# Kernel optimization log

Hardware: AMD Instinct MI355X
Metric: run time of the kernel (lower is better)

Reference implementation:

```python
import jax, jax.numpy as jnp
import numpy as np

N = 50000; E = 320000; DIN = 768; D = 256; R = 4; L = 3
B = 64; T = 6; SD = 128; SH = 256; NC = 14; ALPHA = 0.15
NEG = -1e30


def setup_inputs():
    keys = iter(jax.random.split(jax.random.key(0), 64))
    def nrm(shape, s=0.02):
        return s * jax.random.normal(next(keys), shape, dtype=jnp.float32)
    inp = {}
    inp["x"] = jax.random.normal(next(keys), (N, DIN), dtype=jnp.float32)
    inp["edge_index"] = jax.random.randint(next(keys), (2, E), 0, N)
    inp["edge_type"] = jax.random.randint(next(keys), (E,), 0, R)
    inp["batch"] = jnp.sort(jax.random.randint(next(keys), (N,), 0, B))
    inp["sequence"] = jax.random.normal(next(keys), (B, T, SD), dtype=jnp.float32)
    inp["proj_W"] = nrm((D, DIN)); inp["proj_b"] = nrm((D,))
    inp["Wr"] = nrm((L, R, D, D))
    inp["Ws"] = nrm((L, D, D)); inp["bs"] = nrm((L, D))
    inp["att_W1"] = nrm((L, R, D // 2, 2 * D)); inp["att_b1"] = nrm((L, R, D // 2))
    inp["att_W2"] = nrm((L, R, D // 2)); inp["att_b2"] = nrm((L, R))
    inp["emb"] = nrm((L, R, D // 4), 0.1)
    inp["imp"] = jnp.tile(jnp.array([1.2, 1.1, 1.4, 0.9], dtype=jnp.float32), (L, 1))
    inp["ln_g"] = jnp.ones((L, D), jnp.float32); inp["ln_b"] = jnp.zeros((L, D), jnp.float32)
    inp["gm_W1"] = nrm((D // 2, D)); inp["gm_b1"] = nrm((D // 2,))
    inp["gm_W2"] = nrm((D // 4, D // 2)); inp["gm_b2"] = nrm((D // 4,))
    inp["gm_W3"] = nrm((NC, D // 4)); inp["gm_b3"] = nrm((NC,))
    inp["gru_Wih"] = nrm((2, 3 * SH, SD)); inp["gru_Whh"] = nrm((2, 3 * SH, SH))
    inp["gru_bih"] = nrm((2, 3 * SH)); inp["gru_bhh"] = nrm((2, 3 * SH))
    inp["sm_W1"] = nrm((SH, 2 * SH)); inp["sm_b1"] = nrm((SH,))
    inp["sm_W2"] = nrm((SH // 2, SH)); inp["sm_b2"] = nrm((SH // 2,))
    inp["sm_W3"] = nrm((NC, SH // 2)); inp["sm_b3"] = nrm((NC,))
    return inp


def _gru_dir(x, Wih, Whh, bih, bhh):  # x: [B,T,SD] -> [B,T,SH], torch GRU equations
    def step(h, xt):
        gi = xt @ Wih.T + bih
        gh = h @ Whh.T + bhh
        ir, iz, in_ = jnp.split(gi, 3, axis=-1)
        hr, hz, hn = jnp.split(gh, 3, axis=-1)
        r = jax.nn.sigmoid(ir + hr)
        z = jax.nn.sigmoid(iz + hz)
        n = jnp.tanh(in_ + r * hn)
        h = (1.0 - z) * n + z * h
        return h, h
    h0 = jnp.zeros((x.shape[0], Whh.shape[1]), x.dtype)
    _, ys = jax.lax.scan(step, h0, jnp.swapaxes(x, 0, 1))
    return jnp.swapaxes(ys, 0, 1)


def _gnn_layer(h, h0, src, dst, et, Wr, Ws, bs, aW1, ab1, aW2, ab2, emb, imp, g, b):
    ew = jax.nn.softmax(imp)  # layer_edge_importance softmax over R types
    cat = jnp.concatenate([h[dst], h[src]], axis=1)  # [E, 2D] = [x_i, x_j]
    agg = jnp.zeros_like(h)
    for r in range(R):
        tx = h @ Wr[r].T  # [N, D] per-type transform
        s = jax.nn.relu(cat @ aW1[r].T + ab1[r]) @ aW2[r] + ab2[r]  # [E]
        s = jax.nn.leaky_relu(s, 0.2) + jnp.mean(emb[r])
        mask = et == r
        a = jax.nn.softmax(jnp.where(mask, s, NEG))  # softmax over all type-r edges (dim=0 in torch)
        a = jnp.where(mask, a, 0.0)
        msg = jax.ops.segment_sum(a[:, None] * tx[src], dst, num_segments=h.shape[0])
        agg = agg + ew[r] * msg
    out = (1.0 - ALPHA) * agg + h @ Ws.T + bs + ALPHA * h0
    mu = jnp.mean(out, axis=-1, keepdims=True)
    var = jnp.var(out, axis=-1, keepdims=True)
    out = (out - mu) / jnp.sqrt(var + 1e-5) * g + b  # LayerNorm (eps=1e-5)
    return jax.nn.gelu(out, approximate=False)


def _forward(x, sequence, proj_W, proj_b, Wr, Ws, bs, att_W1, att_b1, att_W2, att_b2, emb, imp, ln_g, ln_b, gm_W1, gm_b1, gm_W2, gm_b2, gm_W3, gm_b3, gru_Wih, gru_Whh, gru_bih, gru_bhh, sm_W1, sm_b1, sm_W2, sm_b2, sm_W3, sm_b3, edge_index, edge_type, batch):
    # sequence branch: bidirectional GRU, avg+max pool over time, MLP readout
    fwd = _gru_dir(sequence, gru_Wih[0], gru_Whh[0], gru_bih[0], gru_bhh[0])
    bwd = _gru_dir(sequence[:, ::-1], gru_Wih[1], gru_Whh[1], gru_bih[1], gru_bhh[1])[:, ::-1]
    seq_out = jnp.concatenate([fwd, bwd], axis=-1)  # [B, T, 2*SH]
    z = jnp.mean(seq_out, axis=1) + jnp.max(seq_out, axis=1)
    z = jax.nn.relu(z @ sm_W1.T + sm_b1)
    z = jax.nn.relu(z @ sm_W2.T + sm_b2)
    seq_logits = z @ sm_W3.T + sm_b3
    # graph branch
    src, dst = edge_index[0], edge_index[1]
    h = x @ proj_W.T + proj_b
    h0 = h
    for i in range(L):
        h = _gnn_layer(h, h0, src, dst, edge_type, Wr[i], Ws[i], bs[i], att_W1[i], att_b1[i], att_W2[i], att_b2[i], emb[i], imp[i], ln_g[i], ln_b[i])
    sums = jax.ops.segment_sum(h, batch, num_segments=B)
    cnt = jax.ops.segment_sum(jnp.ones((h.shape[0],), h.dtype), batch, num_segments=B)
    pooled = sums / jnp.clip(cnt, 1.0)[:, None]  # global_mean_pool
    gz = jax.nn.relu(pooled @ gm_W1.T + gm_b1)
    gz = jax.nn.relu(gz @ gm_W2.T + gm_b2)
    graph_logits = gz @ gm_W3.T + gm_b3
    return graph_logits + seq_logits


def reference(x, edge_index, edge_type, batch, sequence, proj_W, proj_b, Wr, Ws, bs, att_W1, att_b1, att_W2, att_b2, emb, imp, ln_g, ln_b, gm_W1, gm_b1, gm_W2, gm_b2, gm_W3, gm_b3, gru_Wih, gru_Whh, gru_bih, gru_bhh, sm_W1, sm_b1, sm_W2, sm_b2, sm_W3, sm_b3):
    return _forward(x, sequence, proj_W, proj_b, Wr, Ws, bs, att_W1, att_b1, att_W2, att_b2, emb, imp, ln_g, ln_b, gm_W1, gm_b1, gm_W2, gm_b2, gm_W3, gm_b3, gru_Wih, gru_Whh, gru_bih, gru_bhh, sm_W1, sm_b1, sm_W2, sm_b2, sm_W3, sm_b3, edge_index, edge_type, batch)
```

## Files before the change

### kernel.cpp

```cpp
#include <hip/hip_runtime.h>
#include <math.h>

#define N_NODES 50000
#define E_EDGES 320000
#define DIN_    768
#define D_      256
#define R_TYPES 4
#define L_LAYERS 3
#define BATCH_  64
#define T_STEPS 6
#define SD_     128
#define SH_     256
#define NC_     14
#define ALPHA_  0.15f
#define NBLK_B  1250
#define POOL_CHUNK 256
#define E_PAD   (E_EDGES + 256)
#define SCAN_BLK 49

typedef __bf16 bf16_t;
typedef bf16_t bf16x8_t __attribute__((ext_vector_type(8)));
typedef bf16_t bf16x4_t __attribute__((ext_vector_type(4)));
typedef float  f32x4_t  __attribute__((ext_vector_type(4)));

__device__ __forceinline__ f32x4_t mfma16(bf16x8_t a, bf16x8_t b, f32x4_t c) {
    return __builtin_amdgcn_mfma_f32_16x16x32_bf16(a, b, c, 0, 0, 0);
}

__global__ void f2b_kernel(const float* __restrict__ src, bf16_t* __restrict__ dst, int n4)
{
    for (int i = blockIdx.x * blockDim.x + threadIdx.x; i < n4; i += gridDim.x * blockDim.x) {
        float4 v = ((const float4*)src)[i];
        bf16_t o[4] = {(bf16_t)v.x, (bf16_t)v.y, (bf16_t)v.z, (bf16_t)v.w};
        *(ulong1*)&dst[i * 4] = *(ulong1*)o;
    }
}

__global__ void transpose2_kernel(const float* __restrict__ in, float* __restrict__ out, int R, int C)
{
    int total = 2 * R * C;
    for (int i = blockIdx.x * blockDim.x + threadIdx.x; i < total; i += gridDim.x * blockDim.x) {
        int dir = i / (R * C);
        int rem = i - dir * R * C;
        int r = rem / C, c = rem - r * C;
        out[dir * R * C + c * R + r] = in[i];
    }
}

template <bool AF32>
__global__ __launch_bounds__(256) void linear_mfma_t(
    const void* __restrict__ Aptr, const bf16_t* __restrict__ W,
    const float* __restrict__ bias, float* __restrict__ outf,
    bf16_t* __restrict__ outb, int M, int K, int N)
{
    __shared__ bf16_t As[64][40];
    __shared__ bf16_t Bs[64][40];
    const int m0 = blockIdx.x * 64;
    const int n0 = blockIdx.y * 64;
    const int tid = threadIdx.x;
    const int wave = tid >> 6, lane = tid & 63;
    const int wy = wave >> 1, wx = wave & 1;
    const int q = lane >> 4, c = lane & 15;
    const int srow = tid >> 2, skq = tid & 3;

    f32x4_t acc[2][2] = {};
    for (int k0 = 0; k0 < K; k0 += 32) {
        {
            int m = m0 + srow;
            if (AF32) {
                const float* A = (const float*)Aptr;
                bf16_t tmp[8] = {};
                if (m < M) {
                    float4 v0 = *(const float4*)&A[(size_t)m * K + k0 + skq * 8];
                    float4 v1 = *(const float4*)&A[(size_t)m * K + k0 + skq * 8 + 4];
                    tmp[0] = (bf16_t)v0.x; tmp[1] = (bf16_t)v0.y; tmp[2] = (bf16_t)v0.z; tmp[3] = (bf16_t)v0.w;
                    tmp[4] = (bf16_t)v1.x; tmp[5] = (bf16_t)v1.y; tmp[6] = (bf16_t)v1.z; tmp[7] = (bf16_t)v1.w;
                }
                *(bf16x8_t*)&As[srow][skq * 8] = *(bf16x8_t*)tmp;
            } else {
                const bf16_t* A = (const bf16_t*)Aptr;
                bf16x8_t av = {};
                if (m < M) av = *(const bf16x8_t*)&A[(size_t)m * K + k0 + skq * 8];
                *(bf16x8_t*)&As[srow][skq * 8] = av;
            }
            *(bf16x8_t*)&Bs[srow][skq * 8] = *(const bf16x8_t*)&W[(size_t)(n0 + srow) * K + k0 + skq * 8];
        }
        __syncthreads();
        bf16x8_t af[2], bfv[2];
        #pragma unroll
        for (int mt = 0; mt < 2; mt++) af[mt] = *(const bf16x8_t*)&As[wy * 32 + mt * 16 + c][q * 8];
        #pragma unroll
        for (int nt = 0; nt < 2; nt++) bfv[nt] = *(const bf16x8_t*)&Bs[wx * 32 + nt * 16 + c][q * 8];
        #pragma unroll
        for (int mt = 0; mt < 2; mt++)
            #pragma unroll
            for (int nt = 0; nt < 2; nt++)
                acc[mt][nt] = mfma16(af[mt], bfv[nt], acc[mt][nt]);
        __syncthreads();
    }
    #pragma unroll
    for (int mt = 0; mt < 2; mt++) {
        #pragma unroll
        for (int nt = 0; nt < 2; nt++) {
            int n = n0 + wx * 32 + nt * 16 + c;
            float bv = bias ? bias[n] : 0.0f;
            #pragma unroll
            for (int j = 0; j < 4; j++) {
                int m = m0 + wy * 32 + mt * 16 + q * 4 + j;
                if (m < M) {
                    float v = acc[mt][nt][j] + bv;
                    if (outf) outf[(size_t)m * N + n] = v;
                    if (outb) outb[(size_t)m * N + n] = (bf16_t)v;
                }
            }
        }
    }
}

__global__ __launch_bounds__(256) void bucket_count2(const int* __restrict__ et,
                                                     int* __restrict__ blockCnt)
{
    int b = blockIdx.x, tid = threadIdx.x;
    int r = et[b * 256 + tid];
    int lane = tid & 63, wv = tid >> 6;
    __shared__ int wcnt[4][4];
    #pragma unroll
    for (int t = 0; t < 4; t++) {
        unsigned long long m = __ballot(r == t);
        if (lane == 0) wcnt[wv][t] = __popcll(m);
    }
    __syncthreads();
    if (tid < 4)
        blockCnt[b * 4 + tid] = wcnt[0][tid] + wcnt[1][tid] + wcnt[2][tid] + wcnt[3][tid];
}

__global__ void bucket_scan(const int* __restrict__ blockCnt, int* __restrict__ boffP,
                            int* __restrict__ cnt, int* __restrict__ basePerBlock,
                            int* __restrict__ bsrc, int* __restrict__ bdst)
{
    __shared__ int tot[4];
    int t = threadIdx.x;
    if (t < 4) {
        int s = 0;
        for (int b = 0; b < NBLK_B; b++) s += blockCnt[b * 4 + t];
        tot[t] = s;
    }
    __syncthreads();
    if (t == 0) {
        int o = 0;
        for (int r = 0; r < 4; r++) {
            boffP[r] = o; cnt[r] = tot[r];
            o += (tot[r] + 63) & ~63;
        }
        boffP[4] = o;
    }
    __syncthreads();
    if (t < 4) {
        int run = boffP[t];
        for (int b = 0; b < NBLK_B; b++) { basePerBlock[b * 4 + t] = run; run += blockCnt[b * 4 + t]; }
    }
    __syncthreads();
    for (int r = 0; r < 4; r++) {
        int s = boffP[r] + cnt[r], e = boffP[r + 1];
        for (int i = s + t; i < e; i += 64) { bsrc[i] = 0; bdst[i] = 0; }
    }
}

__global__ __launch_bounds__(256) void bucket_scatter2(
    const int* __restrict__ ei, const int* __restrict__ et,
    const int* __restrict__ basePerBlock, int* __restrict__ bsrc, int* __restrict__ bdst)
{
    int b = blockIdx.x, tid = threadIdx.x;
    int e = b * 256 + tid;
    int r = et[e];
    int lane = tid & 63, wv = tid >> 6;
    __shared__ int wcnt[4][4];
    int myrank = 0;
    unsigned long long ltmask = (1ull << lane) - 1ull;
    #pragma unroll
    for (int t = 0; t < 4; t++) {
        unsigned long long m = __ballot(r == t);
        if (r == t) myrank = __popcll(m & ltmask);
        if (lane == 0) wcnt[wv][t] = __popcll(m);
    }
    __syncthreads();
    int wbase = 0;
    for (int w = 0; w < wv; w++) wbase += wcnt[w][r];
    int pos = basePerBlock[b * 4 + r] + wbase + myrank;
    bsrc[pos] = ei[e];
    bdst[pos] = ei[E_EDGES + e];
}

__global__ void embmean_kernel(const float* __restrict__ emb, float* __restrict__ em)
{
    int lr = threadIdx.x;
    if (lr < L_LAYERS * R_TYPES) {
        float s = 0.0f;
        for (int k = 0; k < 64; k++) s += emb[lr * 64 + k];
        em[lr] = s / 64.0f;
    }
}

__global__ __launch_bounds__(256) void deg_count_kernel(
    const int* __restrict__ bdst, const int* __restrict__ boffP, const int* __restrict__ cnt,
    int* __restrict__ deg)
{
    __shared__ int sb[5], sc[4];
    if (threadIdx.x < 5) sb[threadIdx.x] = boffP[threadIdx.x];
    if (threadIdx.x < 4) sc[threadIdx.x] = cnt[threadIdx.x];
    __syncthreads();
    int total = sb[4];
    for (int p = blockIdx.x * blockDim.x + threadIdx.x; p < total; p += gridDim.x * blockDim.x) {
        int r = 0; while (r < 3 && p >= sb[r + 1]) r++;
        if (p - sb[r] < sc[r]) atomicAdd(&deg[bdst[p]], 1);
    }
}

__global__ __launch_bounds__(256) void scan1_kernel(const int* __restrict__ deg,
                                                    int* __restrict__ rowptr, int* __restrict__ blockSum)
{
    __shared__ int sdata[256];
    int b = blockIdx.x, t = threadIdx.x;
    int idx0 = b * 1024 + t * 4;
    int d[4];
    #pragma unroll
    for (int j = 0; j < 4; j++) d[j] = (idx0 + j < N_NODES) ? deg[idx0 + j] : 0;
    int tsum = d[0] + d[1] + d[2] + d[3];
    sdata[t] = tsum;
    __syncthreads();
    for (int off = 1; off < 256; off <<= 1) {
        int v = (t >= off) ? sdata[t - off] : 0;
        __syncthreads();
        sdata[t] += v;
        __syncthreads();
    }
    int ex = sdata[t] - tsum;
    int acc = ex;
    #pragma unroll
    for (int j = 0; j < 4; j++) {
        if (idx0 + j < N_NODES) rowptr[idx0 + j] = acc;
        acc += d[j];
    }
    if (t == 255) blockSum[b] = sdata[255];
}

__global__ void scan2_kernel(const int* __restrict__ blockSum, int* __restrict__ blockOff)
{
    if (threadIdx.x == 0) {
        int o = 0;
        for (int b = 0; b < SCAN_BLK; b++) { blockOff[b] = o; o += blockSum[b]; }
    }
}

__global__ __launch_bounds__(256) void scan3_kernel(int* __restrict__ rowptr,
                                                    const int* __restrict__ blockOff,
                                                    int* __restrict__ cursor)
{
    int idx = blockIdx.x * blockDim.x + threadIdx.x;
    if (idx < N_NODES) {
        int v = rowptr[idx] + blockOff[idx >> 10];
        rowptr[idx] = v; cursor[idx] = v;
    }
    if (idx == 0) rowptr[N_NODES] = E_EDGES;
}

__global__ __launch_bounds__(256) void csr_scatter_kernel(
    const int* __restrict__ bsrc, const int* __restrict__ bdst,
    const int* __restrict__ boffP, const int* __restrict__ cnt,
    int* __restrict__ cursor, int* __restrict__ csrSrc, int* __restrict__ csrPos)
{
    __shared__ int sb[5], sc[4];
    if (threadIdx.x < 5) sb[threadIdx.x] = boffP[threadIdx.x];
    if (threadIdx.x < 4) sc[threadIdx.x] = cnt[threadIdx.x];
    __syncthreads();
    int total = sb[4];
    for (int p = blockIdx.x * blockDim.x + threadIdx.x; p < total; p += gridDim.x * blockDim.x) {
        int r = 0; while (r < 3 && p >= sb[r + 1]) r++;
        if (p - sb[r] < sc[r]) {
            int pos = atomicAdd(&cursor[bdst[p]], 1);
            csrSrc[pos] = bsrc[p];
            csrPos[pos] = p;
        }
    }
}

__global__ __launch_bounds__(256) void attn_mfma(
    const bf16_t* __restrict__ hb, const int* __restrict__ bsrc, const int* __restrict__ bdst,
    const int* __restrict__ boffP, const int* __restrict__ cnt, int l,
    const bf16_t* __restrict__ W1base, const float* __restrict__ b1base,
    const float* __restrict__ W2base, const float* __restrict__ b2base,
    const float* __restrict__ em, float* __restrict__ sbuf)
{
    const int p0 = blockIdx.x * 64;
    if (p0 >= boffP[4]) return;
    int r = 0;
    while (r < 3 && p0 >= boffP[r + 1]) r++;
    const int lr = l * R_TYPES + r;
    const int base = boffP[r];
    const int cnt_r = cnt[r];
    const bf16_t* W1 = W1base + (size_t)lr * 128 * 512;
    const float*  b1 = b1base + lr * 128;
    const float*  W2 = W2base + lr * 128;

    __shared__ int nd_d[64], nd_s[64];
    __shared__ bf16_t Acat[64][40];
    __shared__ bf16_t Bs[128][40];
    const int tid = threadIdx.x;
    if (tid < 64) nd_d[tid] = bdst[p0 + tid];
    else if (tid < 128) nd_s[tid - 64] = bsrc[p0 + tid - 64];
    __syncthreads();
    const int wave = tid >> 6, lane = tid & 63;
    const int q = lane >> 4, c = lane & 15;
    const int srow = tid >> 2, skq = tid & 3;

    f32x4_t acc[8] = {};
    for (int ks = 0; ks < 16; ks++) {
        {
            int node = (ks < 8) ? nd_d[srow] : nd_s[srow];
            int koffm = (ks & 7) * 32 + skq * 8;
            *(bf16x8_t*)&Acat[srow][skq * 8] = *(const bf16x8_t*)&hb[(size_t)node * D_ + koffm];
            #pragma unroll
            for (int s = 0; s < 2; s++) {
                int slot = tid + s * 256;
                int nrow = slot >> 2, nkq = slot & 3;
                *(bf16x8_t*)&Bs[nrow][nkq * 8] = *(const bf16x8_t*)&W1[(size_t)nrow * 512 + ks * 32 + nkq * 8];
            }
        }
        __syncthreads();
        bf16x8_t af = *(const bf16x8_t*)&Acat[wave * 16 + c][q * 8];
        #pragma unroll
        for (int nt = 0; nt < 8; nt++) {
            bf16x8_t bfv = *(const bf16x8_t*)&Bs[nt * 16 + c][q * 8];
            acc[nt] = mfma16(af, bfv, acc[nt]);
        }
        __syncthreads();
    }
    float part[4] = {0, 0, 0, 0};
    #pragma unroll
    for (int nt = 0; nt < 8; nt++) {
        int n = nt * 16 + c;
        float b1v = b1[n], w2v = W2[n];
        #pragma unroll
        for (int j = 0; j < 4; j++) {
            float v = acc[nt][j] + b1v;
            v = v > 0.0f ? v : 0.0f;
            part[j] += v * w2v;
        }
    }
    #pragma unroll
    for (int j = 0; j < 4; j++) {
        #pragma unroll
        for (int mask = 1; mask <= 8; mask <<= 1)
            part[j] += __shfl_xor(part[j], mask);
    }
    if (c == 0) {
        float b2v = b2base[lr], emv = em[lr];
        #pragma unroll
        for (int j = 0; j < 4; j++) {
            int p = p0 + wave * 16 + q * 4 + j;
            bool valid = (p - base) < cnt_r;
            float sv = part[j] + b2v;
            sv = sv > 0.0f ? sv : 0.2f * sv;
            sbuf[p] = valid ? (sv + emv) : -1e30f;
        }
    }
}

__device__ __forceinline__ unsigned fkey(float f) {
    unsigned u = __float_as_uint(f);
    return (u & 0x80000000u) ? ~u : (u | 0x80000000u);
}
__device__ __forceinline__ float fkey_inv(unsigned k) {
    unsigned u = (k & 0x80000000u) ? (k ^ 0x80000000u) : ~k;
    return __uint_as_float(u);
}

__global__ void bucket_max_kernel(const float* __restrict__ sbuf, const int* __restrict__ boffP,
                                  unsigned* __restrict__ redl)
{
    int r = blockIdx.y;
    int lo = boffP[r], hi = boffP[r + 1];
    float m = -1e30f;
    for (int i = lo + blockIdx.x * blockDim.x + threadIdx.x; i < hi; i += gridDim.x * blockDim.x)
        m = fmaxf(m, sbuf[i]);
    for (int o = 32; o; o >>= 1) m = fmaxf(m, __shfl_down(m, o));
    __shared__ float wm[4];
    int lane = threadIdx.x & 63, wv = threadIdx.x >> 6;
    if (lane == 0) wm[wv] = m;
    __syncthreads();
    if (threadIdx.x == 0) {
        float b = fmaxf(fmaxf(wm[0], wm[1]), fmaxf(wm[2], wm[3]));
        atomicMax(&redl[r * 2], fkey(b));
    }
}

__global__ void bucket_sum_kernel(const float* __restrict__ sbuf, const int* __restrict__ boffP,
                                  unsigned* __restrict__ redl)
{
    int r = blockIdx.y;
    int lo = boffP[r], hi = boffP[r + 1];
    float mxf = fkey_inv(redl[r * 2]);
    float s = 0.0f;
    for (int i = lo + blockIdx.x * blockDim.x + threadIdx.x; i < hi; i += gridDim.x * blockDim.x)
        s += expf(sbuf[i] - mxf);
    for (int o = 32; o; o >>= 1) s += __shfl_down(s, o);
    __shared__ float wm[4];
    int lane = threadIdx.x & 63, wv = threadIdx.x >> 6;
    if (lane == 0) wm[wv] = s;
    __syncthreads();
    if (threadIdx.x == 0) atomicAdd((float*)&redl[r * 2 + 1], wm[0] + wm[1] + wm[2] + wm[3]);
}

__global__ __launch_bounds__(256) void msg_ln_gelu_kernel(
    const float* __restrict__ sbuf, const bf16_t* __restrict__ txAll,
    const int* __restrict__ csrSrc, const int* __restrict__ csrPos,
    const int* __restrict__ rowptr, const int* __restrict__ boffP,
    const unsigned* __restrict__ redl, const float* __restrict__ imp, int l,
    const float* __restrict__ accb, const float* __restrict__ h0,
    const float* __restrict__ g, const float* __restrict__ bvec,
    float* __restrict__ h, bf16_t* __restrict__ hb)
{
    __shared__ float smx[4], sinv[4], scoef[4];
    __shared__ int sb[5];
    if (threadIdx.x == 0) {
        float e0 = expf(imp[l * 4 + 0]), e1 = expf(imp[l * 4 + 1]);
        float e2 = expf(imp[l * 4 + 2]), e3 = expf(imp[l * 4 + 3]);
        float den = e0 + e1 + e2 + e3;
        float ews[4] = {e0 / den, e1 / den, e2 / den, e3 / den};
        for (int r = 0; r < 4; r++) {
            smx[r] = fkey_inv(redl[r * 2]);
            sinv[r] = 1.0f / ((const float*)redl)[r * 2 + 1];
            scoef[r] = (1.0f - ALPHA_) * ews[r];
        }
        for (int r = 0; r <= 4; r++) sb[r] = boffP[r];
    }
    __syncthreads();
    int n = blockIdx.x * 4 + (threadIdx.x >> 6);
    if (n >= N_NODES) return;
    int lane = threadIdx.x & 63;
    int c4 = lane * 4;
    float msg[4] = {0, 0, 0, 0};
    int i0 = rowptr[n], i1 = rowptr[n + 1];
    for (int i = i0; i < i1; i++) {
        int src = csrSrc[i];
        int p = csrPos[i];
        int r = 0; while (r < 3 && p >= sb[r + 1]) r++;
        float a = expf(sbuf[p] - smx[r]) * sinv[r] * scoef[r];
        bf16x4_t tv = *(const bf16x4_t*)&txAll[(size_t)src * (R_TYPES * D_) + r * D_ + c4];
        msg[0] += a * (float)tv[0];
        msg[1] += a * (float)tv[1];
        msg[2] += a * (float)tv[2];
        msg[3] += a * (float)tv[3];
    }
    float4 ac = *(const float4*)&accb[(size_t)n * D_ + c4];
    float4 hz = *(const float4*)&h0[(size_t)n * D_ + c4];
    float v[4];
    v[0] = msg[0] + ac.x + ALPHA_ * hz.x;
    v[1] = msg[1] + ac.y + ALPHA_ * hz.y;
    v[2] = msg[2] + ac.z + ALPHA_ * hz.z;
    v[3] = msg[3] + ac.w + ALPHA_ * hz.w;
    float sum = v[0] + v[1] + v[2] + v[3];
    #pragma unroll
    for (int o = 32; o; o >>= 1) sum += __shfl_down(sum, o);
    sum = __shfl(sum, 0);
    float mean = sum * (1.0f / 256.0f);
    float sq = 0.0f;
    #pragma unroll
    for (int j = 0; j < 4; j++) { float d = v[j] - mean; sq += d * d; }
    #pragma unroll
    for (int o = 32; o; o >>= 1) sq += __shfl_down(sq, o);
    sq = __shfl(sq, 0);
    float rstd = rsqrtf(sq * (1.0f / 256.0f) + 1e-5f);
    float4 gg = *(const float4*)&g[c4];
    float4 bb = *(const float4*)&bvec[c4];
    float ga[4] = {gg.x, gg.y, gg.z, gg.w};
    float ba[4] = {bb.x, bb.y, bb.z, bb.w};
    float outv[4];
    bf16_t outb[4];
    #pragma unroll
    for (int j = 0; j < 4; j++) {
        float x = (v[j] - mean) * rstd * ga[j] + ba[j];
        float ge = 0.5f * x * (1.0f + erff(x * 0.7071067811865475f));
        outv[j] = ge;
        outb[j] = (bf16_t)ge;
    }
    *(float4*)&h[(size_t)n * D_ + c4] = *(float4*)outv;
    *(bf16x4_t*)&hb[(size_t)n * D_ + c4] = *(bf16x4_t*)outb;
}

__global__ __launch_bounds__(256) void pool_seg_kernel(
    const float* __restrict__ h, const int* __restrict__ batch,
    float* __restrict__ pooled, float* __restrict__ cntb, int Nn)
{
    int start = blockIdx.x * POOL_CHUNK;
    if (start >= Nn) return;
    int end = start + POOL_CHUNK; if (end > Nn) end = Nn;
    int c = threadIdx.x;
    __shared__ int bseg[POOL_CHUNK];
    if (start + c < Nn) bseg[c] = batch[start + c];
    __syncthreads();
    float acc = 0.0f;
    int cur = bseg[0];
    int segcnt = 0;
    for (int node = start; node < end; node++) {
        int b = bseg[node - start];
        if (b != cur) {
            atomicAdd(&pooled[cur * D_ + c], acc);
            if (c == 0) atomicAdd(&cntb[cur], (float)segcnt);
            acc = 0.0f; segcnt = 0; cur = b;
        }
        acc += h[(size_t)node * D_ + c];
        segcnt++;
    }
    atomicAdd(&pooled[cur * D_ + c], acc);
    if (c == 0) atomicAdd(&cntb[cur], (float)segcnt);
}

__global__ __launch_bounds__(256) void final_mlp_kernel(
    const float* __restrict__ pooled, const float* __restrict__ cntb,
    const float* __restrict__ W1, const float* __restrict__ b1,
    const float* __restrict__ W2, const float* __restrict__ b2,
    const float* __restrict__ W3, const float* __restrict__ b3,
    const float* __restrict__ seqlg, float* __restrict__ out)
{
    int b = blockIdx.x;
    int t = threadIdx.x;
    __shared__ float p[256];
    __shared__ float z1[128];
    __shared__ float z2[64];
    float c = cntb[b]; c = c < 1.0f ? 1.0f : c;
    p[t] = pooled[b * 256 + t] / c;
    __syncthreads();
    if (t < 128) {
        float s = b1[t];
        for (int k = 0; k < 256; k++) s += p[k] * W1[t * 256 + k];
        z1[t] = s > 0.0f ? s : 0.0f;
    }
    __syncthreads();
    if (t < 64) {
        float s = b2[t];
        for (int k = 0; k < 128; k++) s += z1[k] * W2[t * 128 + k];
        z2[t] = s > 0.0f ? s : 0.0f;
    }
    __syncthreads();
    if (t < NC_) {
        float s = b3[t];
        for (int k = 0; k < 64; k++) s += z2[k] * W3[t * 64 + k];
        out[b * NC_ + t] = s + seqlg[b * NC_ + t];
    }
}

__global__ __launch_bounds__(768) void gru_gi_kernel(
    const float* __restrict__ seq, const float* __restrict__ WihT,
    const float* __restrict__ bih, float* __restrict__ gi)
{
    int blk = blockIdx.x;
    int dir = blk >> 6, b = blk & 63;
    __shared__ float xt[T_STEPS * SD_];
    int j = threadIdx.x;
    xt[j] = seq[(size_t)b * T_STEPS * SD_ + j];
    __syncthreads();
    const float* Wt = WihT + (size_t)dir * SD_ * 768;
    float av[T_STEPS] = {};
    for (int k = 0; k < SD_; k++) {
        float w = Wt[(size_t)k * 768 + j];
        #pragma unroll
        for (int t = 0; t < T_STEPS; t++) av[t] += xt[t * SD_ + k] * w;
    }
    float bv = bih[dir * 768 + j];
    for (int t = 0; t < T_STEPS; t++)
        gi[(((size_t)blk) * T_STEPS + t) * 768 + j] = av[t] + bv;
}

__global__ __launch_bounds__(768) void gru_step2(
    const float* __restrict__ gi, const float* __restrict__ WhhT,
    const float* __restrict__ bhh, float* __restrict__ hstate,
    float* __restrict__ outs, int t)
{
    int blk = blockIdx.x;
    int dir = blk >> 6;
    int tin = dir ? (T_STEPS - 1 - t) : t;
    __shared__ float hs[SH_];
    __shared__ float gh[768];
    int j = threadIdx.x;
    if (j < SH_) hs[j] = hstate[(size_t)blk * SH_ + j];
    __syncthreads();
    const float* Wt = WhhT + (size_t)dir * SH_ * 768;
    float a = bhh[dir * 768 + j];
    for (int k = 0; k < SH_; k++)
        a += hs[k] * Wt[(size_t)k * 768 + j];
    gh[j] = a;
    __syncthreads();
    if (j < SH_) {
        size_t gib = (((size_t)blk) * T_STEPS + tin) * 768;
        float r = 1.0f / (1.0f + expf(-(gi[gib + j] + gh[j])));
        float z = 1.0f / (1.0f + expf(-(gi[gib + 256 + j] + gh[256 + j])));
        float n = tanhf(gi[gib + 512 + j] + r * gh[512 + j]);
        float hn = (1.0f - z) * n + z * hs[j];
        hstate[(size_t)blk * SH_ + j] = hn;
        outs[(((size_t)blk) * T_STEPS + tin) * SH_ + j] = hn;
    }
}

__global__ __launch_bounds__(256) void seq_mlp_kernel(
    const float* __restrict__ outs, const float* __restrict__ W1, const float* __restrict__ b1,
    const float* __restrict__ W2, const float* __restrict__ b2,
    const float* __restrict__ W3, const float* __restrict__ b3,
    float* __restrict__ seqlg)
{
    int b = blockIdx.x;
    int t = threadIdx.x;
    __shared__ float z[512];
    __shared__ float z1[256];
    __shared__ float z2[128];
    for (int c = t; c < 512; c += 256) {
        int dir = c >> 8, cc = c & 255;
        float mean = 0.0f, mx = -1e30f;
        for (int tt = 0; tt < T_STEPS; tt++) {
            float v = outs[(((size_t)dir * 64 + b) * T_STEPS + tt) * SH_ + cc];
            mean += v; mx = fmaxf(mx, v);
        }
        z[c] = mean * (1.0f / T_STEPS) + mx;
    }
    __syncthreads();
    {
        float s = b1[t];
        for (int k = 0; k < 512; k++) s += z[k] * W1[t * 512 + k];
        z1[t] = s > 0.0f ? s : 0.0f;
    }
    __syncthreads();
    if (t < 128) {
        float s = b2[t];
        for (int k = 0; k < 256; k++) s += z1[k] * W2[t * 256 + k];
        z2[t] = s > 0.0f ? s : 0.0f;
    }
    __syncthreads();
    if (t < NC_) {
        float s = b3[t];
        for (int k = 0; k < 128; k++) s += z2[k] * W3[t * 128 + k];
        seqlg[b * NC_ + t] = s;
    }
}

extern "C" void kernel_launch(void* const* d_in, const int* in_sizes, int n_in,
                              void* d_out, int out_size, void* d_ws, size_t ws_size,
                              hipStream_t stream)
{
    const float* x      = (const float*)d_in[0];
    const int*   ei     = (const int*)d_in[1];
    const int*   et     = (const int*)d_in[2];
    const int*   batch  = (const int*)d_in[3];
    const float* seq    = (const float*)d_in[4];
    const float* proj_W = (const float*)d_in[5];
    const float* proj_b = (const float*)d_in[6];
    const float* Wr     = (const float*)d_in[7];
    const float* Ws     = (const float*)d_in[8];
    const float* bs     = (const float*)d_in[9];
    const float* aW1    = (const float*)d_in[10];
    const float* ab1    = (const float*)d_in[11];
    const float* aW2    = (const float*)d_in[12];
    const float* ab2    = (const float*)d_in[13];
    const float* emb    = (const float*)d_in[14];
    const float* imp    = (const float*)d_in[15];
    const float* ln_g   = (const float*)d_in[16];
    const float* ln_b   = (const float*)d_in[17];
    const float* gmW1   = (const float*)d_in[18];
    const float* gmb1   = (const float*)d_in[19];
    const float* gmW2   = (const float*)d_in[20];
    const float* gmb2   = (const float*)d_in[21];
    const float* gmW3   = (const float*)d_in[22];
    const float* gmb3   = (const float*)d_in[23];
    const float* gWih   = (const float*)d_in[24];
    const float* gWhh   = (const float*)d_in[25];
    const float* gbih   = (const float*)d_in[26];
    const float* gbhh   = (const float*)d_in[27];
    const float* smW1   = (const float*)d_in[28];
    const float* smb1   = (const float*)d_in[29];
    const float* smW2   = (const float*)d_in[30];
    const float* smb2   = (const float*)d_in[31];
    const float* smW3   = (const float*)d_in[32];
    const float* smb3   = (const float*)d_in[33];
    float* out = (float*)d_out;

    char* ws = (char*)d_ws;
    size_t o = 0;
    auto alloc = [&](size_t bytes) -> void* {
        void* p = ws + o;
        o += (bytes + 1023) & ~(size_t)1023;
        return p;
    };
    float*  h0     = (float*)alloc(sizeof(float) * (size_t)N_NODES * D_);
    float*  h      = (float*)alloc(sizeof(float) * (size_t)N_NODES * D_);
    float*  accb   = (float*)alloc(sizeof(float) * (size_t)N_NODES * D_);
    bf16_t* hbb    = (bf16_t*)alloc(sizeof(bf16_t) * (size_t)N_NODES * D_);
    bf16_t* txAll  = (bf16_t*)alloc(sizeof(bf16_t) * (size_t)N_NODES * R_TYPES * D_);
    bf16_t* projWb = (bf16_t*)alloc(sizeof(bf16_t) * D_ * DIN_);
    bf16_t* Wrb    = (bf16_t*)alloc(sizeof(bf16_t) * L_LAYERS * R_TYPES * D_ * D_);
    bf16_t* Wsb    = (bf16_t*)alloc(sizeof(bf16_t) * L_LAYERS * D_ * D_);
    bf16_t* aW1b   = (bf16_t*)alloc(sizeof(bf16_t) * L_LAYERS * R_TYPES * 128 * 512);
    float*  sbuf   = (float*)alloc(sizeof(float) * E_PAD);
    int*    bsrc   = (int*)alloc(sizeof(int) * E_PAD);
    int*    bdst   = (int*)alloc(sizeof(int) * E_PAD);
    int*    boffP  = (int*)alloc(sizeof(int) * 8);
    int*    cnt    = (int*)alloc(sizeof(int) * 8);
    int*    blockCnt = (int*)alloc(sizeof(int) * NBLK_B * 4);
    int*    basePerBlock = (int*)alloc(sizeof(int) * NBLK_B * 4);
    int*    deg    = (int*)alloc(sizeof(int) * N_NODES);
    int*    rowptr = (int*)alloc(sizeof(int) * (N_NODES + 8));
    int*    cursor = (int*)alloc(sizeof(int) * N_NODES);
    int*    blockSum = (int*)alloc(sizeof(int) * 64);
    int*    blockOff = (int*)alloc(sizeof(int) * 64);
    int*    csrSrc = (int*)alloc(sizeof(int) * E_EDGES);
    int*    csrPos = (int*)alloc(sizeof(int) * E_EDGES);
    unsigned* red  = (unsigned*)alloc(sizeof(unsigned) * 32);
    float*  em     = (float*)alloc(sizeof(float) * 16);
    float*  seqlg  = (float*)alloc(sizeof(float) * BATCH_ * NC_);
    float*  WihT   = (float*)alloc(sizeof(float) * 2 * SD_ * 768);
    float*  WhhT   = (float*)alloc(sizeof(float) * 2 * SH_ * 768);
    float*  gi     = (float*)alloc(sizeof(float) * 2 * BATCH_ * T_STEPS * 768);
    float*  gruH   = (float*)alloc(sizeof(float) * 2 * BATCH_ * SH_);
    float*  gruO   = (float*)alloc(sizeof(float) * 2 * BATCH_ * T_STEPS * SH_);
    float*  pooled = (float*)alloc(sizeof(float) * BATCH_ * D_);
    float*  cntb   = (float*)alloc(sizeof(float) * BATCH_);
    (void)ws_size; (void)in_sizes; (void)n_in; (void)out_size;

    hipMemsetAsync(red, 0, 32 * sizeof(unsigned), stream);
    hipMemsetAsync(gruH, 0, 2 * BATCH_ * SH_ * sizeof(float), stream);
    hipMemsetAsync(pooled, 0, BATCH_ * D_ * sizeof(float), stream);
    hipMemsetAsync(cntb, 0, BATCH_ * sizeof(float), stream);
    hipMemsetAsync(deg, 0, N_NODES * sizeof(int), stream);

    f2b_kernel<<<64, 256, 0, stream>>>(proj_W, projWb, D_ * DIN_ / 4);
    f2b_kernel<<<256, 256, 0, stream>>>(Wr, Wrb, L_LAYERS * R_TYPES * D_ * D_ / 4);
    f2b_kernel<<<64, 256, 0, stream>>>(Ws, Wsb, L_LAYERS * D_ * D_ / 4);
    f2b_kernel<<<256, 256, 0, stream>>>(aW1, aW1b, L_LAYERS * R_TYPES * 128 * 512 / 4);
    transpose2_kernel<<<96, 256, 0, stream>>>(gWih, WihT, 768, SD_);
    transpose2_kernel<<<192, 256, 0, stream>>>(gWhh, WhhT, 768, SH_);

    bucket_count2<<<NBLK_B, 256, 0, stream>>>(et, blockCnt);
    bucket_scan<<<1, 64, 0, stream>>>(blockCnt, boffP, cnt, basePerBlock, bsrc, bdst);
    bucket_scatter2<<<NBLK_B, 256, 0, stream>>>(ei, et, basePerBlock, bsrc, bdst);
    embmean_kernel<<<1, 64, 0, stream>>>(emb, em);

    deg_count_kernel<<<1024, 256, 0, stream>>>(bdst, boffP, cnt, deg);
    scan1_kernel<<<SCAN_BLK, 256, 0, stream>>>(deg, rowptr, blockSum);
    scan2_kernel<<<1, 64, 0, stream>>>(blockSum, blockOff);
    scan3_kernel<<<(N_NODES + 255) / 256, 256, 0, stream>>>(rowptr, blockOff, cursor);
    csr_scatter_kernel<<<1024, 256, 0, stream>>>(bsrc, bdst, boffP, cnt, cursor, csrSrc, csrPos);

    gru_gi_kernel<<<128, 768, 0, stream>>>(seq, WihT, gbih, gi);
    for (int t = 0; t < T_STEPS; t++)
        gru_step2<<<128, 768, 0, stream>>>(gi, WhhT, gbhh, gruH, gruO, t);
    seq_mlp_kernel<<<BATCH_, 256, 0, stream>>>(gruO, smW1, smb1, smW2, smb2, smW3, smb3, seqlg);

    const int MB = (N_NODES + 63) / 64;
    linear_mfma_t<true><<<dim3(MB, D_ / 64), 256, 0, stream>>>(x, projWb, proj_b, h0, hbb, N_NODES, DIN_, D_);
    const int ATTN_BLKS = E_PAD / 64;
    for (int l = 0; l < L_LAYERS; l++) {
        linear_mfma_t<false><<<dim3(MB, D_ / 64), 256, 0, stream>>>(hbb, Wsb + (size_t)l * D_ * D_, bs + l * D_,
                                                                    accb, nullptr, N_NODES, D_, D_);
        linear_mfma_t<false><<<dim3(MB, R_TYPES * D_ / 64), 256, 0, stream>>>(
            hbb, Wrb + (size_t)l * R_TYPES * D_ * D_, nullptr, nullptr, txAll, N_NODES, D_, R_TYPES * D_);
        attn_mfma<<<ATTN_BLKS, 256, 0, stream>>>(hbb, bsrc, bdst, boffP, cnt, l,
                                                 aW1b, ab1, aW2, ab2, em, sbuf);
        bucket_max_kernel<<<dim3(256, 4), 256, 0, stream>>>(sbuf, boffP, red + l * 8);
        bucket_sum_kernel<<<dim3(256, 4), 256, 0, stream>>>(sbuf, boffP, red + l * 8);
        msg_ln_gelu_kernel<<<(N_NODES + 3) / 4, 256, 0, stream>>>(
            sbuf, txAll, csrSrc, csrPos, rowptr, boffP, red + l * 8, imp, l,
            accb, h0, ln_g + l * D_, ln_b + l * D_, h, hbb);
    }

    pool_seg_kernel<<<(N_NODES + POOL_CHUNK - 1) / POOL_CHUNK, 256, 0, stream>>>(h, batch, pooled, cntb, N_NODES);
    final_mlp_kernel<<<BATCH_, 256, 0, stream>>>(pooled, cntb, gmW1, gmb1, gmW2, gmb2, gmW3, gmb3, seqlg, out);
}
```

Baseline: 1.711 ms.

## Merge self and relation GEMMs, widen projection tile, pad LDS rows

After: 1.663 ms. 1.03x faster.

```diff
diff --git a/kernel.cpp b/kernel.cpp
--- a/kernel.cpp
+++ b/kernel.cpp
@@ -17,6 +17,7 @@
 #define POOL_CHUNK 256
 #define E_PAD   (E_EDGES + 256)
 #define SCAN_BLK 49
+#define NCAT    (D_ + R_TYPES * D_)
 
 typedef __bf16 bf16_t;
 typedef bf16_t bf16x8_t __attribute__((ext_vector_type(8)));
@@ -33,6 +34,20 @@
         float4 v = ((const float4*)src)[i];
         bf16_t o[4] = {(bf16_t)v.x, (bf16_t)v.y, (bf16_t)v.z, (bf16_t)v.w};
         *(ulong1*)&dst[i * 4] = *(ulong1*)o;
+    }
+}
+
+__global__ void pack_wcat_kernel(const float* __restrict__ Ws, const float* __restrict__ Wr,
+                                 bf16_t* __restrict__ Wcat)
+{
+    int total = L_LAYERS * NCAT * D_;
+    for (int i = blockIdx.x * blockDim.x + threadIdx.x; i < total; i += gridDim.x * blockDim.x) {
+        int l = i / (NCAT * D_);
+        int rem = i - l * NCAT * D_;
+        int row = rem / D_, k = rem - row * D_;
+        float v = (row < D_) ? Ws[((size_t)l * D_ + row) * D_ + k]
+                             : Wr[((size_t)l * R_TYPES * D_ + (row - D_)) * D_ + k];
+        Wcat[i] = (bf16_t)v;
     }
 }
 
@@ -47,14 +62,76 @@
     }
 }
 
-template <bool AF32>
-__global__ __launch_bounds__(256) void linear_mfma_t(
-    const void* __restrict__ Aptr, const bf16_t* __restrict__ W,
+__global__ __launch_bounds__(256) void proj_mfma(
+    const float* __restrict__ A, const bf16_t* __restrict__ W,
     const float* __restrict__ bias, float* __restrict__ outf,
-    bf16_t* __restrict__ outb, int M, int K, int N)
-{
-    __shared__ bf16_t As[64][40];
-    __shared__ bf16_t Bs[64][40];
+    bf16_t* __restrict__ outb, int M)
+{
+    __shared__ bf16_t As[64][44];
+    __shared__ bf16_t Bs[256][44];
+    const int m0 = blockIdx.x * 64;
+    const int tid = threadIdx.x;
+    const int wave = tid >> 6, lane = tid & 63;
+    const int q = lane >> 4, c = lane & 15;
+    const int srow = tid >> 2, skq = tid & 3;
+
+    f32x4_t acc[4][4] = {};
+    for (int k0 = 0; k0 < DIN_; k0 += 32) {
+        {
+            int m = m0 + srow;
+            bf16_t tmp[8] = {};
+            if (m < M) {
+                float4 v0 = *(const float4*)&A[(size_t)m * DIN_ + k0 + skq * 8];
+                float4 v1 = *(const float4*)&A[(size_t)m * DIN_ + k0 + skq * 8 + 4];
+                tmp[0] = (bf16_t)v0.x; tmp[1] = (bf16_t)v0.y; tmp[2] = (bf16_t)v0.z; tmp[3] = (bf16_t)v0.w;
+                tmp[4] = (bf16_t)v1.x; tmp[5] = (bf16_t)v1.y; tmp[6] = (bf16_t)v1.z; tmp[7] = (bf16_t)v1.w;
+            }
+            *(bf16x8_t*)&As[srow][skq * 8] = *(bf16x8_t*)tmp;
+            #pragma unroll
+            for (int i = 0; i < 4; i++) {
+                int nrow = srow + 64 * i;
+                *(bf16x8_t*)&Bs[nrow][skq * 8] = *(const bf16x8_t*)&W[(size_t)nrow * DIN_ + k0 + skq * 8];
+            }
+        }
+        __syncthreads();
+        bf16x8_t af[4], bfv[4];
+        #pragma unroll
+        for (int mt = 0; mt < 4; mt++) af[mt] = *(const bf16x8_t*)&As[mt * 16 + c][q * 8];
+        #pragma unroll
+        for (int nt = 0; nt < 4; nt++) bfv[nt] = *(const bf16x8_t*)&Bs[wave * 64 + nt * 16 + c][q * 8];
+        #pragma unroll
+        for (int mt = 0; mt < 4; mt++)
+            #pragma unroll
+            for (int nt = 0; nt < 4; nt++)
+                acc[mt][nt] = mfma16(af[mt], bfv[nt], acc[mt][nt]);
+        __syncthreads();
+    }
+    #pragma unroll
+    for (int nt = 0; nt < 4; nt++) {
+        int n = wave * 64 + nt * 16 + c;
+        float bv = bias[n];
+        #pragma unroll
+        for (int mt = 0; mt < 4; mt++) {
+            #pragma unroll
+            for (int j = 0; j < 4; j++) {
+                int m = m0 + mt * 16 + q * 4 + j;
+                if (m < M) {
+                    float v = acc[mt][nt][j] + bv;
+                    outf[(size_t)m * D_ + n] = v;
+                    outb[(size_t)m * D_ + n] = (bf16_t)v;
+                }
+            }
+        }
+    }
+}
+
+__global__ __launch_bounds__(256) void linear_dual_mfma(
+    const bf16_t* __restrict__ A, const bf16_t* __restrict__ W,
+    const float* __restrict__ bias, float* __restrict__ outf,
+    bf16_t* __restrict__ outb, int M)
+{
+    __shared__ bf16_t As[64][44];
+    __shared__ bf16_t Bs[64][44];
     const int m0 = blockIdx.x * 64;
     const int n0 = blockIdx.y * 64;
     const int tid = threadIdx.x;
@@ -64,26 +141,13 @@
     const int srow = tid >> 2, skq = tid & 3;
 
     f32x4_t acc[2][2] = {};
-    for (int k0 = 0; k0 < K; k0 += 32) {
+    for (int k0 = 0; k0 < D_; k0 += 32) {
         {
             int m = m0 + srow;
-            if (AF32) {
-                const float* A = (const float*)Aptr;
-                bf16_t tmp[8] = {};
-                if (m < M) {
-                    float4 v0 = *(const float4*)&A[(size_t)m * K + k0 + skq * 8];
-                    float4 v1 = *(const float4*)&A[(size_t)m * K + k0 + skq * 8 + 4];
-                    tmp[0] = (bf16_t)v0.x; tmp[1] = (bf16_t)v0.y; tmp[2] = (bf16_t)v0.z; tmp[3] = (bf16_t)v0.w;
-                    tmp[4] = (bf16_t)v1.x; tmp[5] = (bf16_t)v1.y; tmp[6] = (bf16_t)v1.z; tmp[7] = (bf16_t)v1.w;
-                }
-                *(bf16x8_t*)&As[srow][skq * 8] = *(bf16x8_t*)tmp;
-            } else {
-                const bf16_t* A = (const bf16_t*)Aptr;
-                bf16x8_t av = {};
-                if (m < M) av = *(const bf16x8_t*)&A[(size_t)m * K + k0 + skq * 8];
-                *(bf16x8_t*)&As[srow][skq * 8] = av;
-            }
-            *(bf16x8_t*)&Bs[srow][skq * 8] = *(const bf16x8_t*)&W[(size_t)(n0 + srow) * K + k0 + skq * 8];
+            bf16x8_t av = {};
+            if (m < M) av = *(const bf16x8_t*)&A[(size_t)m * D_ + k0 + skq * 8];
+            *(bf16x8_t*)&As[srow][skq * 8] = av;
+            *(bf16x8_t*)&Bs[srow][skq * 8] = *(const bf16x8_t*)&W[(size_t)(n0 + srow) * D_ + k0 + skq * 8];
         }
         __syncthreads();
         bf16x8_t af[2], bfv[2];
@@ -103,14 +167,14 @@
         #pragma unroll
         for (int nt = 0; nt < 2; nt++) {
             int n = n0 + wx * 32 + nt * 16 + c;
-            float bv = bias ? bias[n] : 0.0f;
+            float bv = (n < D_) ? bias[n] : 0.0f;
             #pragma unroll
             for (int j = 0; j < 4; j++) {
                 int m = m0 + wy * 32 + mt * 16 + q * 4 + j;
                 if (m < M) {
                     float v = acc[mt][nt][j] + bv;
-                    if (outf) outf[(size_t)m * N + n] = v;
-                    if (outb) outb[(size_t)m * N + n] = (bf16_t)v;
+                    if (n < D_) outf[(size_t)m * D_ + n] = v;
+                    else        outb[(size_t)m * (R_TYPES * D_) + (n - D_)] = (bf16_t)v;
                 }
             }
         }
@@ -303,8 +367,8 @@
     const float*  W2 = W2base + lr * 128;
 
     __shared__ int nd_d[64], nd_s[64];
-    __shared__ bf16_t Acat[64][40];
-    __shared__ bf16_t Bs[128][40];
+    __shared__ bf16_t Acat[64][44];
+    __shared__ bf16_t Bs[128][44];
     const int tid = threadIdx.x;
     if (tid < 64) nd_d[tid] = bdst[p0 + tid];
     else if (tid < 128) nd_s[tid - 64] = bsrc[p0 + tid - 64];
@@ -695,8 +759,7 @@
     bf16_t* hbb    = (bf16_t*)alloc(sizeof(bf16_t) * (size_t)N_NODES * D_);
     bf16_t* txAll  = (bf16_t*)alloc(sizeof(bf16_t) * (size_t)N_NODES * R_TYPES * D_);
     bf16_t* projWb = (bf16_t*)alloc(sizeof(bf16_t) * D_ * DIN_);
-    bf16_t* Wrb    = (bf16_t*)alloc(sizeof(bf16_t) * L_LAYERS * R_TYPES * D_ * D_);
-    bf16_t* Wsb    = (bf16_t*)alloc(sizeof(bf16_t) * L_LAYERS * D_ * D_);
+    bf16_t* Wcat   = (bf16_t*)alloc(sizeof(bf16_t) * L_LAYERS * NCAT * D_);
     bf16_t* aW1b   = (bf16_t*)alloc(sizeof(bf16_t) * L_LAYERS * R_TYPES * 128 * 512);
     float*  sbuf   = (float*)alloc(sizeof(float) * E_PAD);
     int*    bsrc   = (int*)alloc(sizeof(int) * E_PAD);
@@ -731,8 +794,7 @@
     hipMemsetAsync(deg, 0, N_NODES * sizeof(int), stream);
 
     f2b_kernel<<<64, 256, 0, stream>>>(proj_W, projWb, D_ * DIN_ / 4);
-    f2b_kernel<<<256, 256, 0, stream>>>(Wr, Wrb, L_LAYERS * R_TYPES * D_ * D_ / 4);
-    f2b_kernel<<<64, 256, 0, stream>>>(Ws, Wsb, L_LAYERS * D_ * D_ / 4);
+    pack_wcat_kernel<<<512, 256, 0, stream>>>(Ws, Wr, Wcat);
     f2b_kernel<<<256, 256, 0, stream>>>(aW1, aW1b, L_LAYERS * R_TYPES * 128 * 512 / 4);
     transpose2_kernel<<<96, 256, 0, stream>>>(gWih, WihT, 768, SD_);
     transpose2_kernel<<<192, 256, 0, stream>>>(gWhh, WhhT, 768, SH_);
@@ -754,13 +816,11 @@
     seq_mlp_kernel<<<BATCH_, 256, 0, stream>>>(gruO, smW1, smb1, smW2, smb2, smW3, smb3, seqlg);
 
     const int MB = (N_NODES + 63) / 64;
-    linear_mfma_t<true><<<dim3(MB, D_ / 64), 256, 0, stream>>>(x, projWb, proj_b, h0, hbb, N_NODES, DIN_, D_);
+    proj_mfma<<<MB, 256, 0, stream>>>(x, projWb, proj_b, h0, hbb, N_NODES);
     const int ATTN_BLKS = E_PAD / 64;
     for (int l = 0; l < L_LAYERS; l++) {
-        linear_mfma_t<false><<<dim3(MB, D_ / 64), 256, 0, stream>>>(hbb, Wsb + (size_t)l * D_ * D_, bs + l * D_,
-                                                                    accb, nullptr, N_NODES, D_, D_);
-        linear_mfma_t<false><<<dim3(MB, R_TYPES * D_ / 64), 256, 0, stream>>>(
-            hbb, Wrb + (size_t)l * R_TYPES * D_ * D_, nullptr, nullptr, txAll, N_NODES, D_, R_TYPES * D_);
+        linear_dual_mfma<<<dim3(MB, NCAT / 64), 256, 0, stream>>>(
+            hbb, Wcat + (size_t)l * NCAT * D_, bs + l * D_, accb, txAll, N_NODES);
         attn_mfma<<<ATTN_BLKS, 256, 0, stream>>>(hbb, bsrc, bdst, boffP, cnt, l,
                                                  aW1b, ab1, aW2, ab2, em, sbuf);
         bucket_max_kernel<<<dim3(256, 4), 256, 0, stream>>>(sbuf, boffP, red + l * 8);
```
